# Performance work log

Hardware: AMD Instinct MI355X
Metric: run time of the kernel (lower is better)

The kernel has to match this reference:

```python
import jax, jax.numpy as jnp
import numpy as np

D_MODEL = 2048
NUM_HEADS = 16
NUM_GROUPS = 4
HEAD_DIM = D_MODEL // NUM_HEADS
ROPE_THETA = 10000.0


def apply_rope(x):
    # x: [B, S, H, Dh]; positions = arange(S); interleaved-pair rotary
    B, S, H, Dh = x.shape
    inv_freq = 1.0 / (ROPE_THETA ** (jnp.arange(0, Dh, 2, dtype=jnp.float32) / Dh))  # [Dh/2]
    pos = jnp.arange(S, dtype=jnp.float32)
    ang = pos[:, None] * inv_freq[None, :]            # [S, Dh/2]
    cos = jnp.cos(ang)[None, :, None, :]              # [1, S, 1, Dh/2]
    sin = jnp.sin(ang)[None, :, None, :]
    x1 = x[..., 0::2]
    x2 = x[..., 1::2]
    r1 = x1 * cos - x2 * sin
    r2 = x1 * sin + x2 * cos
    return jnp.stack([r1, r2], axis=-1).reshape(B, S, H, Dh)


def setup_inputs() -> dict:
    key = jax.random.key(0)
    kx, kq, kk, kv, ko = jax.random.split(key, 5)
    B, S = 4, 4096
    x = jax.random.normal(kx, (B, S, D_MODEL), dtype=jnp.float32)
    init = 0.02
    Wq = jax.random.normal(kq, (D_MODEL, D_MODEL), dtype=jnp.float32) * init
    Wk = jax.random.normal(kk, (D_MODEL, D_MODEL), dtype=jnp.float32) * init
    Wv = jax.random.normal(kv, (D_MODEL, D_MODEL), dtype=jnp.float32) * init
    Wo = jax.random.normal(ko, (D_MODEL, D_MODEL), dtype=jnp.float32) * init
    return {"x": x, "Wq": Wq, "Wk": Wk, "Wv": Wv, "Wo": Wo}


def reference(x, Wq, Wk, Wv, Wo):
    B, S, _ = x.shape
    H, G, Dh = NUM_HEADS, NUM_GROUPS, HEAD_DIM
    q = (x @ Wq.T).reshape(B, S, H, Dh)
    k = (x @ Wk.T).reshape(B, S, H, Dh)
    v = (x @ Wv.T).reshape(B, S, H, Dh)
    q = apply_rope(q)
    k = apply_rope(k)
    # GQA head permutation: (B,S,G,H/G,Dh) -> transpose(2,3) -> (B,S,H,Dh)
    q = q.reshape(B, S, G, H // G, Dh).transpose(0, 1, 3, 2, 4).reshape(B, S, H, Dh)
    # NOTE: faithful to source — scores are over the HEAD axis: [B,S,H,H]
    scores = jnp.einsum("bshd,bstd->bsht", q, k) / jnp.sqrt(jnp.asarray(Dh, x.dtype))
    probs = jax.nn.softmax(scores, axis=-1)
    attn = jnp.einsum("bsht,bstd->bshd", probs, v).reshape(B, S, H * Dh)
    return attn @ Wo.T
```

## Files before the change

kernel.cpp:

```cpp
#include <hip/hip_runtime.h>
#include <hip/hip_bf16.h>
#include <stdint.h>


typedef __attribute__((ext_vector_type(8))) short short8;
typedef __attribute__((ext_vector_type(4))) float f32x4;
typedef uint16_t u16;

typedef __attribute__((address_space(1))) const void as1_const_void;
typedef __attribute__((address_space(3))) void as3_void;
#define GLD_LDS16(gp, lp)                                                     \
  __builtin_amdgcn_global_load_lds((as1_const_void*)(gp), (as3_void*)(lp),    \
                                   16, 0, 0)

__device__ __forceinline__ float bf2f(u16 u) {
  uint32_t x = ((uint32_t)u) << 16;
  float f;
  __builtin_memcpy(&f, &x, 4);
  return f;
}
__device__ __forceinline__ u16 f2bf(float f) {
  uint32_t u;
  __builtin_memcpy(&u, &f, 4);
  u += 0x7fffu + ((u >> 16) & 1u);
  return (u16)(u >> 16);
}

__global__ __launch_bounds__(256) void cvt_f32_to_bf16_v4(
    const float* __restrict__ s, u16* __restrict__ d, int n4) {
  int i = blockIdx.x * 256 + threadIdx.x;
  if (i >= n4) return;
  const float4 v = reinterpret_cast<const float4*>(s)[i];
  ushort4 o;
  o.x = f2bf(v.x);
  o.y = f2bf(v.y);
  o.z = f2bf(v.z);
  o.w = f2bf(v.w);
  reinterpret_cast<ushort4*>(d)[i] = o;
}

template <int OUT_F32>
__global__ __launch_bounds__(256, 2) void gemm_bt(
    const u16* __restrict__ A, const u16* __restrict__ B,
    void* __restrict__ Cout, int M, int N, int K) {
  __shared__ u16 sA[128 * 64];
  __shared__ u16 sB[128 * 64];
  const int tid = threadIdx.x;
  const int lane = tid & 63;
  const int wid = tid >> 6;
  const int m0 = blockIdx.y * 128;
  const int n0 = blockIdx.x * 128;
  const int wr = wid >> 1, wc = wid & 1;

  f32x4 acc[4][4];
#pragma unroll
  for (int i = 0; i < 4; ++i)
#pragma unroll
    for (int j = 0; j < 4; ++j) acc[i][j] = {0.f, 0.f, 0.f, 0.f};

  const int nK = K >> 6;
  for (int kt = 0; kt < nK; ++kt) {
    const u16* Ag = A + (size_t)m0 * K + kt * 64;
    const u16* Bg = B + (size_t)n0 * K + kt * 64;
#pragma unroll
    for (int it = 0; it < 4; ++it) {
      const int o = (it * 256 + tid) * 16;
      const int row = o >> 7;
      const int colb = o & 127;
      GLD_LDS16((const char*)(Ag + (size_t)row * K) + colb,
                (char*)sA + it * 4096 + wid * 1024);
    }
#pragma unroll
    for (int it = 0; it < 4; ++it) {
      const int o = (it * 256 + tid) * 16;
      const int row = o >> 7;
      const int colb = o & 127;
      GLD_LDS16((const char*)(Bg + (size_t)row * K) + colb,
                (char*)sB + it * 4096 + wid * 1024);
    }
    __syncthreads();

#pragma unroll
    for (int kk = 0; kk < 2; ++kk) {
      short8 af[4], bfr[4];
      const int col = kk * 32 + (lane >> 4) * 8;
#pragma unroll
      for (int f = 0; f < 4; ++f) {
        const int ra = wr * 64 + f * 16 + (lane & 15);
        af[f] = *reinterpret_cast<const short8*>(&sA[ra * 64 + col]);
        const int rb = wc * 64 + f * 16 + (lane & 15);
        bfr[f] = *reinterpret_cast<const short8*>(&sB[rb * 64 + col]);
      }
#pragma unroll
      for (int i = 0; i < 4; ++i)
#pragma unroll
        for (int j = 0; j < 4; ++j)
          acc[i][j] = __builtin_amdgcn_mfma_f32_16x16x32_bf16(
              af[i], bfr[j], acc[i][j], 0, 0, 0);
    }
    __syncthreads();
  }

  const int rbase = m0 + wr * 64 + ((lane >> 4) << 2);
  const int cbase = n0 + wc * 64 + (lane & 15);
  if (OUT_F32) {
    float* C = (float*)Cout;
#pragma unroll
    for (int i = 0; i < 4; ++i)
#pragma unroll
      for (int j = 0; j < 4; ++j)
#pragma unroll
        for (int e = 0; e < 4; ++e)
          C[(size_t)(rbase + i * 16 + e) * N + (cbase + j * 16)] =
              acc[i][j][e];
  } else {
    u16* C = (u16*)Cout;
#pragma unroll
    for (int i = 0; i < 4; ++i)
#pragma unroll
      for (int j = 0; j < 4; ++j)
#pragma unroll
        for (int e = 0; e < 4; ++e)
          C[(size_t)(rbase + i * 16 + e) * N + (cbase + j * 16)] =
              f2bf(acc[i][j][e]);
  }
}

__global__ __launch_bounds__(256) void rope_attn(
    const u16* __restrict__ qkv, u16* __restrict__ attn, int S) {
  __shared__ float cosv[64], sinv[64];
  __shared__ float sq[16][132];
  __shared__ float sk[16][132];
  __shared__ float sp[16][16];
  const int token = blockIdx.x;
  const int s = token & (S - 1);
  const int tid = threadIdx.x;
  const u16* base = qkv + (size_t)token * 6144;

  if (tid < 64) {
    const float inv = powf(10000.0f, -(float)tid * (1.0f / 64.0f));
    float sv, cv;
    sincosf((float)s * inv, &sv, &cv);
    cosv[tid] = cv;
    sinv[tid] = sv;
  }
  __syncthreads();

#pragma unroll
  for (int p = 0; p < 8; ++p) {
    const int idx = p * 256 + tid;
    const int mat = idx >> 10;
    const int rem = idx & 1023;
    const int h = rem >> 6;
    const int i = rem & 63;
    const u16* src = base + mat * 2048 + h * 128 + 2 * i;
    const float x1 = bf2f(src[0]);
    const float x2 = bf2f(src[1]);
    const float c = cosv[i], sn = sinv[i];
    float* dst = mat ? sk[h] : sq[h];
    dst[2 * i] = x1 * c - x2 * sn;
    dst[2 * i + 1] = x1 * sn + x2 * c;
  }
  __syncthreads();

  {
    const int h = tid >> 4;
    const int t = tid & 15;
    const int hp = ((h & 3) << 2) | (h >> 2);
    float sc = 0.f;
#pragma unroll
    for (int d = 0; d < 128; ++d) sc += sq[hp][d] * sk[t][d];
    sc *= 0.08838834764831845f;
    float mx = sc;
#pragma unroll
    for (int o = 8; o; o >>= 1) mx = fmaxf(mx, __shfl_xor(mx, o, 16));
    const float e = __expf(sc - mx);
    float sum = e;
#pragma unroll
    for (int o = 8; o; o >>= 1) sum += __shfl_xor(sum, o, 16);
    sp[h][t] = e / sum;
  }
  __syncthreads();

  {
    const int h = tid >> 4;
    const int d0 = (tid & 15) * 8;
    const u16* vb = base + 4096;
    float o[8] = {0.f, 0.f, 0.f, 0.f, 0.f, 0.f, 0.f, 0.f};
#pragma unroll
    for (int t = 0; t < 16; ++t) {
      const float pr = sp[h][t];
      const short8 vv = *reinterpret_cast<const short8*>(vb + t * 128 + d0);
#pragma unroll
      for (int e = 0; e < 8; ++e) o[e] += pr * bf2f((u16)vv[e]);
    }
    short8 ov;
#pragma unroll
    for (int e = 0; e < 8; ++e) ov[e] = (short)f2bf(o[e]);
    *reinterpret_cast<short8*>(attn + (size_t)token * 2048 + h * 128 + d0) =
        ov;
  }
}

extern "C" void kernel_launch(void* const* d_in, const int* in_sizes, int n_in,
                              void* d_out, int out_size, void* d_ws,
                              size_t ws_size, hipStream_t stream) {
  (void)in_sizes;
  (void)n_in;
  (void)out_size;
  (void)ws_size;
  const float* x = (const float*)d_in[0];
  const float* Wq = (const float*)d_in[1];
  const float* Wk = (const float*)d_in[2];
  const float* Wv = (const float*)d_in[3];
  const float* Wo = (const float*)d_in[4];
  float* out = (float*)d_out;

  const int B = 4, S = 4096, D = 2048;
  const int M = B * S;

  char* ws = (char*)d_ws;
  u16* xb = (u16*)ws;
  u16* wqkv = (u16*)(ws + (size_t)M * D * 2);
  u16* wo = (u16*)((char*)wqkv + (size_t)3 * D * D * 2);
  u16* qkv = (u16*)((char*)wo + (size_t)D * D * 2);

  cvt_f32_to_bf16_v4<<<(M * D / 4 + 255) / 256, 256, 0, stream>>>(x, xb,
                                                                  M * D / 4);
  const int w4 = D * D / 4;
  cvt_f32_to_bf16_v4<<<(w4 + 255) / 256, 256, 0, stream>>>(Wq, wqkv, w4);
  cvt_f32_to_bf16_v4<<<(w4 + 255) / 256, 256, 0, stream>>>(
      Wk, wqkv + (size_t)D * D, w4);
  cvt_f32_to_bf16_v4<<<(w4 + 255) / 256, 256, 0, stream>>>(
      Wv, wqkv + (size_t)2 * D * D, w4);
  cvt_f32_to_bf16_v4<<<(w4 + 255) / 256, 256, 0, stream>>>(Wo, wo, w4);

  gemm_bt<0><<<dim3(3 * D / 128, M / 128), 256, 0, stream>>>(xb, wqkv, qkv, M,
                                                             3 * D, D);
  rope_attn<<<M, 256, 0, stream>>>(qkv, xb, S);
  gemm_bt<1><<<dim3(D / 128, M / 128), 256, 0, stream>>>(xb, wo, out, M, D, D);
}
```

Baseline: 806.5 us.

## Replace GEMM with 256x256-tile, double-buffered, swizzled-LDS pipelined kernel

Replaces the 128x128 single-buffered GEMM with a 256x256-tile, 512-thread kernel. It double-buffers 128 KB of dynamic LDS and interleaves global-to-LDS prefetch of the next K-tile with MFMA work using explicit waitcnt and barriers. It also XOR-swizzles LDS to avoid bank conflicts, remaps workgroups across XCDs for L2 locality, and raises MFMA priority with setprio. The aim is to hide memory latency and raise arithmetic intensity in both projection GEMMs, at the cost of higher register and LDS pressure and fragile hand-written synchronisation.

```diff
diff --git a/kernel.cpp b/kernel.cpp
--- a/kernel.cpp
+++ b/kernel.cpp
@@ -9,9 +9,26 @@
 
 typedef __attribute__((address_space(1))) const void as1_const_void;
 typedef __attribute__((address_space(3))) void as3_void;
+
 #define GLD_LDS16(gp, lp)                                                     \
   __builtin_amdgcn_global_load_lds((as1_const_void*)(gp), (as3_void*)(lp),    \
                                    16, 0, 0)
+
+#define BAR() asm volatile("s_barrier" ::: "memory")
+#define LGKM0()                                            \
+  {                                                        \
+    asm volatile("s_waitcnt lgkmcnt(0)" ::: "memory");     \
+    __builtin_amdgcn_sched_barrier(0);                     \
+  }
+#define VMCNT(n) asm volatile("s_waitcnt vmcnt(" #n ")" ::: "memory")
+
+__device__ __forceinline__ short8 ds_read_b128p(const char* p) {
+  short8 r;
+  const __attribute__((address_space(3))) char* lp =
+      (const __attribute__((address_space(3))) char*)p;
+  asm volatile("ds_read_b128 %0, %1" : "=v"(r) : "v"(lp));
+  return r;
+}
 
 __device__ __forceinline__ float bf2f(u16 u) {
   uint32_t x = ((uint32_t)u) << 16;
@@ -40,88 +57,182 @@
 }
 
 template <int OUT_F32>
-__global__ __launch_bounds__(256, 2) void gemm_bt(
+__global__ __launch_bounds__(512, 2) void gemm256(
     const u16* __restrict__ A, const u16* __restrict__ B,
     void* __restrict__ Cout, int M, int N, int K) {
-  __shared__ u16 sA[128 * 64];
-  __shared__ u16 sB[128 * 64];
+  extern __shared__ char smem[];
   const int tid = threadIdx.x;
   const int lane = tid & 63;
   const int wid = tid >> 6;
-  const int m0 = blockIdx.y * 128;
-  const int n0 = blockIdx.x * 128;
-  const int wr = wid >> 1, wc = wid & 1;
-
-  f32x4 acc[4][4];
-#pragma unroll
-  for (int i = 0; i < 4; ++i)
-#pragma unroll
-    for (int j = 0; j < 4; ++j) acc[i][j] = {0.f, 0.f, 0.f, 0.f};
-
-  const int nK = K >> 6;
-  for (int kt = 0; kt < nK; ++kt) {
-    const u16* Ag = A + (size_t)m0 * K + kt * 64;
-    const u16* Bg = B + (size_t)n0 * K + kt * 64;
-#pragma unroll
-    for (int it = 0; it < 4; ++it) {
-      const int o = (it * 256 + tid) * 16;
+  const int wr = wid >> 2;
+  const int wc = wid & 3;
+  const int lr = lane & 15;
+  const int kq = lane >> 4;
+
+  const int nwg = gridDim.x * gridDim.y;
+  const int orig = blockIdx.y * gridDim.x + blockIdx.x;
+  const int qq = nwg >> 3, rr = nwg & 7;
+  const int xcd = orig & 7, loc = orig >> 3;
+  const int wg =
+      (xcd < rr ? xcd * (qq + 1) : rr * (qq + 1) + (xcd - rr) * qq) + loc;
+  const int m0 = (wg / gridDim.x) * 256;
+  const int n0 = (wg % gridDim.x) * 256;
+
+  const int nt = K >> 6;
+
+  auto stage = [&](int bsel, int hidx, int kt) {
+    char* base = smem + bsel * 65536 + hidx * 16384;
+    const u16* G = (hidx >= 2) ? A : B;
+    const int rowbase = (hidx >= 2) ? (m0 + (hidx - 2) * 128) : (n0 + hidx * 128);
+#pragma unroll
+    for (int it = 0; it < 2; ++it) {
+      const int o = it * 8192 + tid * 16;
       const int row = o >> 7;
-      const int colb = o & 127;
-      GLD_LDS16((const char*)(Ag + (size_t)row * K) + colb,
-                (char*)sA + it * 4096 + wid * 1024);
-    }
-#pragma unroll
-    for (int it = 0; it < 4; ++it) {
-      const int o = (it * 256 + tid) * 16;
-      const int row = o >> 7;
-      const int colb = o & 127;
-      GLD_LDS16((const char*)(Bg + (size_t)row * K) + colb,
-                (char*)sB + it * 4096 + wid * 1024);
-    }
-    __syncthreads();
-
-#pragma unroll
-    for (int kk = 0; kk < 2; ++kk) {
-      short8 af[4], bfr[4];
-      const int col = kk * 32 + (lane >> 4) * 8;
-#pragma unroll
-      for (int f = 0; f < 4; ++f) {
-        const int ra = wr * 64 + f * 16 + (lane & 15);
-        af[f] = *reinterpret_cast<const short8*>(&sA[ra * 64 + col]);
-        const int rb = wc * 64 + f * 16 + (lane & 15);
-        bfr[f] = *reinterpret_cast<const short8*>(&sB[rb * 64 + col]);
+      const int lch = ((o >> 4) & 7) ^ (row & 7);
+      GLD_LDS16(G + (size_t)(rowbase + row) * K + (size_t)kt * 64 + lch * 8,
+                base + it * 8192 + wid * 1024);
+    }
+  };
+  auto frag = [&](const char* half, int row, int kk) {
+    const uint32_t L = (uint32_t)(row * 128 + (kk * 4 + kq) * 16);
+    return ds_read_b128p(half + (L ^ (((uint32_t)row & 7) << 4)));
+  };
+
+  f32x4 acc[8][4];
+#pragma unroll
+  for (int i = 0; i < 8; ++i)
+#pragma unroll
+    for (int j = 0; j < 4; ++j) acc[i][j] = (f32x4){0.f, 0.f, 0.f, 0.f};
+
+  stage(0, 0, 0);
+  stage(0, 1, 0);
+  stage(0, 2, 0);
+  stage(0, 3, 0);
+  stage(1, 0, 1);
+  stage(1, 1, 1);
+  stage(1, 2, 1);
+  VMCNT(6);
+  BAR();
+
+  int cur = 0;
+#pragma unroll 2
+  for (int t = 0; t < nt; ++t, cur ^= 1) {
+    const char* Ah = smem + cur * 65536 + 32768 + wr * 16384;
+    const char* Bh = smem + cur * 65536 + (wc >> 1) * 16384;
+    short8 a0[4][2], a1[4][2], b0[2][2], b1[2][2];
+
+#pragma unroll
+    for (int f = 0; f < 4; ++f) {
+      const int row = f * 16 + lr;
+      a0[f][0] = frag(Ah, row, 0);
+      a0[f][1] = frag(Ah, row, 1);
+    }
+#pragma unroll
+    for (int j = 0; j < 2; ++j) {
+      const int row = (wc & 1) * 64 + j * 16 + lr;
+      b0[j][0] = frag(Bh, row, 0);
+      b0[j][1] = frag(Bh, row, 1);
+    }
+    if (t + 1 < nt) stage(cur ^ 1, 3, t + 1);
+    BAR();
+    LGKM0();
+    __builtin_amdgcn_s_setprio(1);
+#pragma unroll
+    for (int i = 0; i < 4; ++i)
+#pragma unroll
+      for (int j = 0; j < 2; ++j) {
+        acc[i][j] = __builtin_amdgcn_mfma_f32_16x16x32_bf16(
+            a0[i][0], b0[j][0], acc[i][j], 0, 0, 0);
+        acc[i][j] = __builtin_amdgcn_mfma_f32_16x16x32_bf16(
+            a0[i][1], b0[j][1], acc[i][j], 0, 0, 0);
       }
-#pragma unroll
-      for (int i = 0; i < 4; ++i)
-#pragma unroll
-        for (int j = 0; j < 4; ++j)
-          acc[i][j] = __builtin_amdgcn_mfma_f32_16x16x32_bf16(
-              af[i], bfr[j], acc[i][j], 0, 0, 0);
-    }
-    __syncthreads();
-  }
-
-  const int rbase = m0 + wr * 64 + ((lane >> 4) << 2);
-  const int cbase = n0 + wc * 64 + (lane & 15);
+    __builtin_amdgcn_s_setprio(0);
+    BAR();
+
+#pragma unroll
+    for (int f = 0; f < 4; ++f) {
+      const int row = (4 + f) * 16 + lr;
+      a1[f][0] = frag(Ah, row, 0);
+      a1[f][1] = frag(Ah, row, 1);
+    }
+#pragma unroll
+    for (int j = 0; j < 2; ++j) {
+      const int row = (wc & 1) * 64 + (2 + j) * 16 + lr;
+      b1[j][0] = frag(Bh, row, 0);
+      b1[j][1] = frag(Bh, row, 1);
+    }
+    BAR();
+    LGKM0();
+    __builtin_amdgcn_s_setprio(1);
+#pragma unroll
+    for (int i = 0; i < 4; ++i)
+#pragma unroll
+      for (int j = 0; j < 2; ++j) {
+        acc[i][2 + j] = __builtin_amdgcn_mfma_f32_16x16x32_bf16(
+            a0[i][0], b1[j][0], acc[i][2 + j], 0, 0, 0);
+        acc[i][2 + j] = __builtin_amdgcn_mfma_f32_16x16x32_bf16(
+            a0[i][1], b1[j][1], acc[i][2 + j], 0, 0, 0);
+      }
+    __builtin_amdgcn_s_setprio(0);
+    BAR();
+
+    if (t + 2 < nt) {
+      stage(cur, 0, t + 2);
+      stage(cur, 1, t + 2);
+    }
+    __builtin_amdgcn_s_setprio(1);
+#pragma unroll
+    for (int i = 0; i < 4; ++i)
+#pragma unroll
+      for (int j = 0; j < 2; ++j) {
+        acc[4 + i][j] = __builtin_amdgcn_mfma_f32_16x16x32_bf16(
+            a1[i][0], b0[j][0], acc[4 + i][j], 0, 0, 0);
+        acc[4 + i][j] = __builtin_amdgcn_mfma_f32_16x16x32_bf16(
+            a1[i][1], b0[j][1], acc[4 + i][j], 0, 0, 0);
+      }
+    __builtin_amdgcn_s_setprio(0);
+    BAR();
+
+    if (t + 2 < nt) stage(cur, 2, t + 2);
+    __builtin_amdgcn_s_setprio(1);
+#pragma unroll
+    for (int i = 0; i < 4; ++i)
+#pragma unroll
+      for (int j = 0; j < 2; ++j) {
+        acc[4 + i][2 + j] = __builtin_amdgcn_mfma_f32_16x16x32_bf16(
+            a1[i][0], b1[j][0], acc[4 + i][2 + j], 0, 0, 0);
+        acc[4 + i][2 + j] = __builtin_amdgcn_mfma_f32_16x16x32_bf16(
+            a1[i][1], b1[j][1], acc[4 + i][2 + j], 0, 0, 0);
+      }
+    __builtin_amdgcn_s_setprio(0);
+    if (t + 2 < nt) {
+      VMCNT(6);
+    } else if (t + 1 < nt) {
+      VMCNT(0);
+    }
+    BAR();
+  }
+
+  const int rb = m0 + wr * 128 + (kq << 2);
+  const int cb = n0 + wc * 64 + lr;
   if (OUT_F32) {
     float* C = (float*)Cout;
 #pragma unroll
-    for (int i = 0; i < 4; ++i)
+    for (int i = 0; i < 8; ++i)
 #pragma unroll
       for (int j = 0; j < 4; ++j)
 #pragma unroll
         for (int e = 0; e < 4; ++e)
-          C[(size_t)(rbase + i * 16 + e) * N + (cbase + j * 16)] =
-              acc[i][j][e];
+          C[(size_t)(rb + i * 16 + e) * N + (cb + j * 16)] = acc[i][j][e];
   } else {
     u16* C = (u16*)Cout;
 #pragma unroll
-    for (int i = 0; i < 4; ++i)
+    for (int i = 0; i < 8; ++i)
 #pragma unroll
       for (int j = 0; j < 4; ++j)
 #pragma unroll
         for (int e = 0; e < 4; ++e)
-          C[(size_t)(rbase + i * 16 + e) * N + (cbase + j * 16)] =
+          C[(size_t)(rb + i * 16 + e) * N + (cb + j * 16)] =
               f2bf(acc[i][j][e]);
   }
 }
@@ -225,6 +336,11 @@
   u16* wo = (u16*)((char*)wqkv + (size_t)3 * D * D * 2);
   u16* qkv = (u16*)((char*)wo + (size_t)D * D * 2);
 
+  hipFuncSetAttribute(reinterpret_cast<const void*>(&gemm256<0>),
+                      hipFuncAttributeMaxDynamicSharedMemorySize, 131072);
+  hipFuncSetAttribute(reinterpret_cast<const void*>(&gemm256<1>),
+                      hipFuncAttributeMaxDynamicSharedMemorySize, 131072);
+
   cvt_f32_to_bf16_v4<<<(M * D / 4 + 255) / 256, 256, 0, stream>>>(x, xb,
                                                                   M * D / 4);
   const int w4 = D * D / 4;
@@ -235,8 +351,9 @@
       Wv, wqkv + (size_t)2 * D * D, w4);
   cvt_f32_to_bf16_v4<<<(w4 + 255) / 256, 256, 0, stream>>>(Wo, wo, w4);
 
-  gemm_bt<0><<<dim3(3 * D / 128, M / 128), 256, 0, stream>>>(xb, wqkv, qkv, M,
-                                                             3 * D, D);
+  gemm256<0><<<dim3(3 * D / 256, M / 256), 512, 131072, stream>>>(
+      xb, wqkv, qkv, M, 3 * D, D);
   rope_attn<<<M, 256, 0, stream>>>(qkv, xb, S);
-  gemm_bt<1><<<dim3(D / 128, M / 128), 256, 0, stream>>>(xb, wo, out, M, D, D);
-}
+  gemm256<1><<<dim3(D / 256, M / 256), 512, 131072, stream>>>(xb, wo, out, M,
+                                                              D, D);
+}
```

Result: slower. 983.1 us (+21.9%).
